# Kernel optimization log

Measured on AMD Instinct MI355X. Metric: run time of the kernel, lower is better.

Reference implementation:

```python
import jax, jax.numpy as jnp
import numpy as np

N_THRESH = 100  # thresholds = 0.00, 0.01, ..., 0.99


def setup_inputs() -> dict:
    key = jax.random.key(0)
    k1, k2 = jax.random.split(key)
    predicted_mask = jax.random.uniform(k1, (32, 1, 1024, 1024), dtype=jnp.float32)
    gt_mask = jax.random.randint(k2, (32, 1, 1024, 1024), 0, 2, dtype=jnp.int32)
    return {"predicted_mask": predicted_mask, "gt_mask": gt_mask}


def reference(predicted_mask, gt_mask):
    # Single-pass histogram formulation of: for each t_k in arange(0,1,0.01),
    # iou_k = |(pred > t_k) & gt| / |(pred > t_k) | gt|  (torchmetrics binary Jaccard,
    # strict '>' thresholding, safe-divide -> 0 when union is empty).
    thresholds = jnp.arange(0.0, 1.0, 0.01, dtype=jnp.float32)  # [100], sorted
    pred = jnp.squeeze(predicted_mask).ravel()                  # [N] probabilities in [0,1]
    gt = jnp.squeeze(gt_mask).ravel().astype(jnp.float32)       # [N] 0/1

    # cnt[i] = number of thresholds strictly below pred[i]; pixel i satisfies
    # (pred > t_k) exactly for k in [0, cnt[i]).
    cnt = jnp.searchsorted(thresholds, pred, side='left')       # [N] int in [0, 100]

    hist_pos = jax.ops.segment_sum(gt, cnt, num_segments=N_THRESH + 1)              # [101]
    hist_all = jax.ops.segment_sum(jnp.ones_like(gt), cnt, num_segments=N_THRESH + 1)

    # TP_k = #{pred > t_k and gt==1} = sum_{c > k} hist_pos[c]  (suffix sums via cumsum)
    tp = jnp.sum(hist_pos) - jnp.cumsum(hist_pos)[:N_THRESH]        # [100]
    pred_pos = jnp.sum(hist_all) - jnp.cumsum(hist_all)[:N_THRESH]  # [100] #{pred > t_k}
    n_gt_pos = jnp.sum(gt)

    union = pred_pos + n_gt_pos - tp                                 # TP + FP + FN
    ious = jnp.where(union > 0, tp / jnp.maximum(union, 1.0), 0.0)   # safe divide -> 0
    return thresholds, ious
```

## Files before the change

### kernel.cpp

```cpp
#include <hip/hip_runtime.h>

#define N_THRESH 100
#define NBINS 101
#define TPB 256
#define GRID 256

__global__ void zero_ws_kernel(unsigned long long* __restrict__ ws) {
    int i = threadIdx.x;
    if (i < NBINS + 1) ws[i] = 0ull;
}

__device__ __forceinline__ int bin_of(float v) {
    int e = (int)(v * 100.0f);
    e = e < 0 ? 0 : (e > 99 ? 99 : e);
    double ed = (double)e * 0.01;
    float t0 = (float)ed;
    float t1 = (float)(ed + 0.01);
    int c = e + (t0 < v ? 1 : 0) + (t1 < v ? 1 : 0);
    return c > N_THRESH ? N_THRESH : c;
}

__device__ __forceinline__ void bump(unsigned int* __restrict__ h, int tid,
                                     float v, int g) {
    h[bin_of(v) * TPB + tid] += 1u + ((unsigned int)(g != 0) << 16);
}

#define PROCESS16(PA, PB, PC, PD, GA, GB, GC, GD) do {          \
    bump(h, tid, (PA).x, (GA).x); bump(h, tid, (PA).y, (GA).y); \
    bump(h, tid, (PA).z, (GA).z); bump(h, tid, (PA).w, (GA).w); \
    bump(h, tid, (PB).x, (GB).x); bump(h, tid, (PB).y, (GB).y); \
    bump(h, tid, (PB).z, (GB).z); bump(h, tid, (PB).w, (GB).w); \
    bump(h, tid, (PC).x, (GC).x); bump(h, tid, (PC).y, (GC).y); \
    bump(h, tid, (PC).z, (GC).z); bump(h, tid, (PC).w, (GC).w); \
    bump(h, tid, (PD).x, (GD).x); bump(h, tid, (PD).y, (GD).y); \
    bump(h, tid, (PD).z, (GD).z); bump(h, tid, (PD).w, (GD).w); \
} while (0)

__global__ __launch_bounds__(TPB) void hist_kernel(
        const float* __restrict__ pred,
        const int* __restrict__ gt,
        unsigned long long* __restrict__ ws,
        float* __restrict__ out,
        int n) {
    __shared__ unsigned int hist[NBINS][TPB];
    __shared__ unsigned int fpos[NBINS], fall[NBINS];
    __shared__ int is_last;

    const int tid = threadIdx.x;
    unsigned int* const h = &hist[0][0];

    for (int i = tid; i < NBINS * TPB; i += TPB) h[i] = 0u;
    __syncthreads();

    const int nvec = n >> 2;
    const float4* __restrict__ p4 = (const float4*)pred;
    const int4*   __restrict__ g4 = (const int4*)gt;
    const int gsz = gridDim.x * blockDim.x;
    const int i0  = blockIdx.x * blockDim.x + tid;
    const int iters  = nvec / gsz;
    const int groups = iters >> 2;

    int it = 0;
    if (groups > 0) {
        int j = i0;
        float4 pa = p4[j], pb = p4[j + gsz], pc = p4[j + 2 * gsz], pd = p4[j + 3 * gsz];
        int4   ga = g4[j], gb = g4[j + gsz], gc = g4[j + 2 * gsz], gd = g4[j + 3 * gsz];
        for (int g = 1; g < groups; ++g) {
            j = i0 + g * 4 * gsz;
            float4 qa = p4[j], qb = p4[j + gsz], qc = p4[j + 2 * gsz], qd = p4[j + 3 * gsz];
            int4   ra = g4[j], rb = g4[j + gsz], rc = g4[j + 2 * gsz], rd = g4[j + 3 * gsz];
            PROCESS16(pa, pb, pc, pd, ga, gb, gc, gd);
            pa = qa; pb = qb; pc = qc; pd = qd;
            ga = ra; gb = rb; gc = rc; gd = rd;
        }
        PROCESS16(pa, pb, pc, pd, ga, gb, gc, gd);
        it = groups * 4;
    }
    for (; it < iters; ++it) {
        int i = i0 + it * gsz;
        float4 p = p4[i]; int4 g = g4[i];
        bump(h, tid, p.x, g.x); bump(h, tid, p.y, g.y);
        bump(h, tid, p.z, g.z); bump(h, tid, p.w, g.w);
    }
    {
        int i = i0 + iters * gsz;
        if (i < nvec) {
            float4 p = p4[i]; int4 g = g4[i];
            bump(h, tid, p.x, g.x); bump(h, tid, p.y, g.y);
            bump(h, tid, p.z, g.z); bump(h, tid, p.w, g.w);
        }
    }

    if (blockIdx.x == 0 && tid == 0) {
        for (int k = nvec << 2; k < n; ++k)
            h[bin_of(pred[k]) * TPB] += 1u + ((unsigned int)(gt[k] != 0) << 16);
    }

    __syncthreads();
    if (tid < NBINS) {
        const unsigned int* row = &hist[tid][0];
        unsigned long long cnt = 0ull, pos = 0ull;
        for (int j = 0; j < TPB; ++j) {
            int jj = j + tid; if (jj >= TPB) jj -= TPB;
            unsigned int v = row[jj];
            cnt += v & 0xffffu;
            pos += v >> 16;
        }
        if (cnt | pos) atomicAdd(&ws[tid], (pos << 32) | cnt);
        __threadfence();
    }
    __syncthreads();
    if (tid == 0) {
        unsigned long long t = atomicAdd(&ws[NBINS], 1ull);
        is_last = (t == (unsigned long long)(gridDim.x - 1)) ? 1 : 0;
    }
    __syncthreads();

    if (is_last) {
        if (tid < NBINS) {
            unsigned long long hv = atomicAdd(&ws[tid], 0ull);
            fpos[tid] = (unsigned int)(hv >> 32);
            fall[tid] = (unsigned int)(hv & 0xffffffffull);
        }
        __syncthreads();
        if (tid < N_THRESH) {
            out[tid] = (float)((double)tid * 0.01);
            unsigned long long tp = 0, pp = 0, ngt = 0;
            for (int c = tid + 1; c <= N_THRESH; ++c) { tp += fpos[c]; pp += fall[c]; }
            for (int c = 0; c <= N_THRESH; ++c) ngt += fpos[c];
            long long uni = (long long)(pp + ngt - tp);
            double iou = (uni > 0) ? (double)tp / (double)uni : 0.0;
            out[N_THRESH + tid] = (float)iou;
        }
    }
}

extern "C" void kernel_launch(void* const* d_in, const int* in_sizes, int n_in,
                              void* d_out, int out_size, void* d_ws, size_t ws_size,
                              hipStream_t stream) {
    const float* pred = (const float*)d_in[0];
    const int*   gt   = (const int*)d_in[1];
    float* out = (float*)d_out;
    unsigned long long* ws = (unsigned long long*)d_ws;
    int n = in_sizes[0];

    zero_ws_kernel<<<1, 128, 0, stream>>>(ws);
    hist_kernel<<<GRID, TPB, 0, stream>>>(pred, gt, ws, out, n);
}
```

Baseline: 295.5 us.

## Replace per-thread LDS histograms with shared pair-binned 2D atomic histogram

```diff
diff --git a/kernel.cpp b/kernel.cpp
--- a/kernel.cpp
+++ b/kernel.cpp
@@ -2,6 +2,7 @@
 
 #define N_THRESH 100
 #define NBINS 101
+#define NCOL 102
 #define TPB 256
 #define GRID 256
 
@@ -20,20 +21,24 @@
     return c > N_THRESH ? N_THRESH : c;
 }
 
-__device__ __forceinline__ void bump(unsigned int* __restrict__ h, int tid,
-                                     float v, int g) {
-    h[bin_of(v) * TPB + tid] += 1u + ((unsigned int)(g != 0) << 16);
+__device__ __forceinline__ void bump_pair(unsigned long long* __restrict__ c,
+                                          float va, int ga, float vb, int gb) {
+    int a = bin_of(va), b = bin_of(vb);
+    unsigned long long contrib = 1ull
+        | ((unsigned long long)(ga != 0) << 20)
+        | ((unsigned long long)(gb != 0) << 40);
+    atomicAdd(&c[a * NCOL + b], contrib);
 }
 
-#define PROCESS16(PA, PB, PC, PD, GA, GB, GC, GD) do {          \
-    bump(h, tid, (PA).x, (GA).x); bump(h, tid, (PA).y, (GA).y); \
-    bump(h, tid, (PA).z, (GA).z); bump(h, tid, (PA).w, (GA).w); \
-    bump(h, tid, (PB).x, (GB).x); bump(h, tid, (PB).y, (GB).y); \
-    bump(h, tid, (PB).z, (GB).z); bump(h, tid, (PB).w, (GB).w); \
-    bump(h, tid, (PC).x, (GC).x); bump(h, tid, (PC).y, (GC).y); \
-    bump(h, tid, (PC).z, (GC).z); bump(h, tid, (PC).w, (GC).w); \
-    bump(h, tid, (PD).x, (GD).x); bump(h, tid, (PD).y, (GD).y); \
-    bump(h, tid, (PD).z, (GD).z); bump(h, tid, (PD).w, (GD).w); \
+#define PROCESS16(PA, PB, PC, PD, GA, GB, GC, GD) do {                 \
+    bump_pair(cells, (PA).x, (GA).x, (PA).y, (GA).y);                  \
+    bump_pair(cells, (PA).z, (GA).z, (PA).w, (GA).w);                  \
+    bump_pair(cells, (PB).x, (GB).x, (PB).y, (GB).y);                  \
+    bump_pair(cells, (PB).z, (GB).z, (PB).w, (GB).w);                  \
+    bump_pair(cells, (PC).x, (GC).x, (PC).y, (GC).y);                  \
+    bump_pair(cells, (PC).z, (GC).z, (PC).w, (GC).w);                  \
+    bump_pair(cells, (PD).x, (GD).x, (PD).y, (GD).y);                  \
+    bump_pair(cells, (PD).z, (GD).z, (PD).w, (GD).w);                  \
 } while (0)
 
 __global__ __launch_bounds__(TPB) void hist_kernel(
@@ -42,14 +47,16 @@
         unsigned long long* __restrict__ ws,
         float* __restrict__ out,
         int n) {
-    __shared__ unsigned int hist[NBINS][TPB];
+    __shared__ unsigned long long cells[NBINS * NCOL];
     __shared__ unsigned int fpos[NBINS], fall[NBINS];
     __shared__ int is_last;
 
     const int tid = threadIdx.x;
-    unsigned int* const h = &hist[0][0];
 
-    for (int i = tid; i < NBINS * TPB; i += TPB) h[i] = 0u;
+    {
+        unsigned int* z = (unsigned int*)cells;
+        for (int i = tid; i < NBINS * NCOL * 2; i += TPB) z[i] = 0u;
+    }
     __syncthreads();
 
     const int nvec = n >> 2;
@@ -79,32 +86,39 @@
     for (; it < iters; ++it) {
         int i = i0 + it * gsz;
         float4 p = p4[i]; int4 g = g4[i];
-        bump(h, tid, p.x, g.x); bump(h, tid, p.y, g.y);
-        bump(h, tid, p.z, g.z); bump(h, tid, p.w, g.w);
+        bump_pair(cells, p.x, g.x, p.y, g.y);
+        bump_pair(cells, p.z, g.z, p.w, g.w);
     }
     {
         int i = i0 + iters * gsz;
         if (i < nvec) {
             float4 p = p4[i]; int4 g = g4[i];
-            bump(h, tid, p.x, g.x); bump(h, tid, p.y, g.y);
-            bump(h, tid, p.z, g.z); bump(h, tid, p.w, g.w);
+            bump_pair(cells, p.x, g.x, p.y, g.y);
+            bump_pair(cells, p.z, g.z, p.w, g.w);
         }
     }
 
     if (blockIdx.x == 0 && tid == 0) {
-        for (int k = nvec << 2; k < n; ++k)
-            h[bin_of(pred[k]) * TPB] += 1u + ((unsigned int)(gt[k] != 0) << 16);
+        for (int k = nvec << 2; k < n; ++k) {
+            unsigned long long contrib = 1ull
+                | ((unsigned long long)(gt[k] != 0) << 20);
+            cells[bin_of(pred[k]) * NCOL + NBINS] += contrib;
+        }
     }
 
     __syncthreads();
     if (tid < NBINS) {
-        const unsigned int* row = &hist[tid][0];
         unsigned long long cnt = 0ull, pos = 0ull;
-        for (int j = 0; j < TPB; ++j) {
-            int jj = j + tid; if (jj >= TPB) jj -= TPB;
-            unsigned int v = row[jj];
-            cnt += v & 0xffffu;
-            pos += v >> 16;
+        const unsigned long long* row = &cells[tid * NCOL];
+        for (int j = 0; j < NCOL; ++j) {
+            unsigned long long v = row[j];
+            cnt += v & 0xFFFFFull;
+            pos += (v >> 20) & 0xFFFFFull;
+        }
+        for (int i = 0; i < NBINS; ++i) {
+            unsigned long long v = cells[i * NCOL + tid];
+            cnt += v & 0xFFFFFull;
+            pos += (v >> 40) & 0xFFFFFull;
         }
         if (cnt | pos) atomicAdd(&ws[tid], (pos << 32) | cnt);
         __threadfence();
```

New measurement: 287.9 us. -2.6%, faster.
